# Kernel optimization log

Measured on AMD Instinct MI355X. Metric: run time of the kernel, lower is better.

Reference implementation:

```python
import jax, jax.numpy as jnp
import numpy as np

N, F, T, E = 20000, 128, 4, 640000
TBL = 10002  # oscillator lookup: indices 0..10001 (clamped inputs map to 10001)
EPS = 1e-5


def setup_inputs() -> dict:
    key = jax.random.key(0)
    ks = jax.random.split(key, 12)
    rn = lambda k, shp, s: (jax.random.normal(k, shp, dtype=jnp.float32) * s)
    return {
        "x": rn(ks[0], (N, F), 1.0),
        "osc_table": jax.random.uniform(ks[1], (TBL,), dtype=jnp.float32),
        "edge_index": jax.random.randint(ks[2], (2, E), 0, N, dtype=jnp.int32),
        "edge_type": jax.random.randint(ks[3], (E,), 0, T, dtype=jnp.int32),
        "w_ih": rn(ks[4], (4 * F, F), 0.05),
        "w_hh": rn(ks[5], (4 * F, F), 0.05),
        "b_ih": jnp.zeros((4 * F,), jnp.float32),
        "b_hh": jnp.zeros((4 * F,), jnp.float32),
        "conv1_w": rn(ks[6], (T, 2 * F, F), 0.001),
        "conv1_b": jnp.zeros((2 * F,), jnp.float32),
        "conv2_w": rn(ks[7], (T, F, 2 * F), 0.001),
        "conv2_b": jnp.zeros((F,), jnp.float32),
        "lin1_w": rn(ks[8], (2 * F, F), 0.05),
        "lin1_b": jnp.zeros((2 * F,), jnp.float32),
        "lin2_w": rn(ks[9], (F, 2 * F), 0.05),
        "lin2_b": jnp.zeros((F,), jnp.float32),
        "bn1_g": jnp.ones((2 * F,), jnp.float32),
        "bn1_b": jnp.zeros((2 * F,), jnp.float32),
        "bn2_g": jnp.ones((F,), jnp.float32),
        "bn2_b": jnp.zeros((F,), jnp.float32),
    }


def _oscillator(x, table):
    # clamp out-of-range inputs to 0.5001 -> index 10001
    xi = jnp.where((x < -0.5) | (x > 0.5), jnp.float32(0.5001), x)
    idx = jnp.floor((xi + 0.5) * 10000.0).astype(jnp.int32)
    vals = table[idx]
    # where table value is 0, fall back to Sig'(original input) = sigmoid(x) (s=1)
    return jnp.where(vals == 0, jax.nn.sigmoid(x), vals)


def _ec_conv(x, W, b, src, dst, etype):
    # per-edge-type scatter-MAX aggregation, vectorized via composite segment ids
    msgs = x[src]                                  # [E, Cin]
    seg = dst * T + etype                          # [E]
    agg = jax.ops.segment_max(msgs, seg, num_segments=N * T)  # [N*T, Cin]
    agg = jnp.where(jnp.isfinite(agg), agg, 0.0)   # empty segments (-inf) -> 0 (PyG zero-fill)
    agg = agg.reshape(N, T, -1)
    # sum_t linear(agg_t, W_t, b) ; bias is added once per edge type in the torch loop
    return jnp.einsum("ntc,toc->no", agg, W) + T * b


def _batchnorm(x, gamma, beta):
    mu = jnp.mean(x, axis=0)
    var = jnp.mean((x - mu) ** 2, axis=0)          # biased variance (training mode)
    return (x - mu) * jax.lax.rsqrt(var + EPS) * gamma + beta


def reference(x, osc_table, edge_index, edge_type, w_ih, w_hh, b_ih, b_hh,
              conv1_w, conv1_b, conv2_w, conv2_b, lin1_w, lin1_b, lin2_w, lin2_b,
              bn1_g, bn1_b, bn2_g, bn2_b):
    src, dst = edge_index[0], edge_index[1]
    h = _oscillator(x, osc_table)
    # LSTM over a length-1 sequence (unsqueeze(0), batch_first=False) with zero state:
    gates = h @ w_ih.T + b_ih + b_hh               # h0=0 so w_hh contributes nothing
    i, f, g, o = jnp.split(gates, 4, axis=-1)
    c = jax.nn.sigmoid(i) * jnp.tanh(g)
    h = jax.nn.sigmoid(o) * jnp.tanh(c)
    h = h @ lin1_w.T + lin1_b + _ec_conv(h, conv1_w, conv1_b, src, dst, edge_type)
    h = jax.nn.relu(_batchnorm(h, bn1_g, bn1_b))
    h = h @ lin2_w.T + lin2_b + _ec_conv(h, conv2_w, conv2_b, src, dst, edge_type)
    h = _batchnorm(h, bn2_g, bn2_b)
    return jax.nn.sigmoid(h - 10.0)
```

## Files before the change

### kernel.cpp

```cpp
#include <hip/hip_runtime.h>
#include <math.h>

#define NN 20000
#define NE 640000
#define TT 4
#define FF 128
#define FF2 256
#define NSEG (NN*TT)
#define MP 20096
#define NBUCK 157
#define EPSBN 1e-5f

typedef short bf16x8 __attribute__((ext_vector_type(8)));
typedef float f32x4  __attribute__((ext_vector_type(4)));
typedef unsigned short us2 __attribute__((ext_vector_type(2)));

__device__ __forceinline__ float sigf(float x){ return 1.0f/(1.0f+expf(-x)); }

__device__ __forceinline__ unsigned short f2bf(float x){
  union { float f; unsigned u; } v; v.f = x;
  unsigned r = v.u + 0x7FFF + ((v.u >> 16) & 1);
  return (unsigned short)(r >> 16);
}
__device__ __forceinline__ float bf2f(unsigned short u){
  union { float f; unsigned u; } v; v.u = ((unsigned)u) << 16; return v.f;
}

__device__ __forceinline__ unsigned char f2f8(float x){
  union{float f; unsigned u;} v; v.f = x;
  unsigned s = (v.u >> 24) & 0x80u;
  unsigned a = v.u & 0x7FFFFFFFu;
  if(a > 0x43E00000u) a = 0x43E00000u;
  union{unsigned u; float f;} w; w.u = a;
  float ax = w.f;
  if(ax < 0.015625f){
    int q = (int)rintf(ax * 512.0f);
    return (unsigned char)(s | (unsigned)q);
  }
  unsigned rb = a & 0xFFFFFu;
  unsigned base = a >> 20;
  unsigned r = base + (((rb > 0x80000u) || (rb == 0x80000u && (base & 1u))) ? 1u : 0u);
  unsigned e = r >> 3, m3 = r & 7u;
  int fe = (int)e - 120;
  if(fe >= 16) return (unsigned char)(s | 0x7Eu);
  return (unsigned char)(s | ((unsigned)fe << 3) | m3);
}
__device__ __forceinline__ unsigned char fold8(unsigned char b){
  return (unsigned char)(b ^ ((b & 0x80u) ? 0xFFu : 0x80u));
}
__device__ __forceinline__ unsigned short key8tobf(unsigned char k){
  unsigned char b = (unsigned char)(k ^ ((k & 0x80u) ? 0x80u : 0xFFu));
  unsigned s = ((unsigned)b & 0x80u) << 24;
  unsigned e = ((unsigned)b >> 3) & 0xFu;
  unsigned m = (unsigned)b & 7u;
  union{unsigned u; float f;} v;
  if(e == 0){ v.f = (float)m * 0.001953125f; v.u |= s; }
  else v.u = s | ((e + 120u) << 23) | (m << 20);
  return (unsigned short)(v.u >> 16);
}
__device__ __forceinline__ void acc8(unsigned v, unsigned &me, unsigned &mo){
  union U{unsigned u; us2 v;};
  U a, b, r;
  a.u = __builtin_amdgcn_perm(v, 0u, 0x0C060C04u);
  b.u = me; r.v = __builtin_elementwise_max(a.v, b.v); me = r.u;
  a.u = __builtin_amdgcn_perm(v, 0u, 0x0C070C05u);
  b.u = mo; r.v = __builtin_elementwise_max(a.v, b.v); mo = r.u;
}
__device__ __forceinline__ unsigned maxsplit(unsigned a, unsigned b){
  union U{unsigned u; us2 v;};
  U x, y, r; x.u = a; y.u = b;
  r.v = __builtin_elementwise_max(x.v, y.v);
  return r.u;
}

#define PB0 147456
#define PB1 (PB0 + 229376)
#define PB2 (PB1 + 229376)
__global__ __launch_bounds__(256)
void k_prep(const float* __restrict__ w_ih, const float* __restrict__ lin1_w,
            const float* __restrict__ conv1_w, const float* __restrict__ lin2_w,
            const float* __restrict__ conv2_w,
            const float* __restrict__ bih, const float* __restrict__ bhh,
            const float* __restrict__ l1b, const float* __restrict__ c1b,
            const float* __restrict__ l2b, const float* __restrict__ c2b,
            unsigned short* __restrict__ Bp0, unsigned short* __restrict__ Bp1,
            unsigned short* __restrict__ Bp2,
            float* __restrict__ bias0, float* __restrict__ bias1, float* __restrict__ bias2,
            int* __restrict__ gbcnt, int* __restrict__ gcursor,
            float* __restrict__ bnsum1, float* __restrict__ bnsum2){
  int gi = blockIdx.x*256 + threadIdx.x;
  if(gi < PB0){
    int k = gi/384, o = gi - k*384;
    int grow = (o < 128) ? o : o + 128;
    int reg = k >> 7, c = k & 127;
    float w = w_ih[(size_t)grow*128 + c];
    unsigned short hu = f2bf(w);
    Bp0[((size_t)(k >> 3)*384 + o)*8 + (k & 7)] = (reg == 1) ? f2bf(w - bf2f(hu)) : hu;
  } else if(gi < PB1){
    int i = gi - PB0; int k = i >> 8, o = i & 255;
    int reg = k >> 7;
    unsigned short val;
    if(reg < 3){
      float w = lin1_w[(size_t)o*128 + (k & 127)];
      unsigned short hu = f2bf(w);
      val = (reg == 1) ? f2bf(w - bf2f(hu)) : hu;
    } else {
      int kk = k - 384; int t = kk >> 7; int c = kk & 127;
      val = f2bf(conv1_w[((size_t)t*256 + o)*128 + c]);
    }
    Bp1[((size_t)(k >> 3)*256 + o)*8 + (k & 7)] = val;
  } else if(gi < PB2){
    int i = gi - PB1; int k = i >> 7, o = i & 127;
    int reg = k >> 8;
    unsigned short val;
    if(reg < 3){
      float w = lin2_w[(size_t)o*256 + (k & 255)];
      unsigned short hu = f2bf(w);
      val = (reg == 1) ? f2bf(w - bf2f(hu)) : hu;
    } else {
      int kk = k - 768; int t = kk >> 8; int c = kk & 255;
      val = f2bf(conv2_w[((size_t)t*128 + o)*256 + c]);
    }
    Bp2[((size_t)(k >> 3)*128 + o)*8 + (k & 7)] = val;
  } else {
    int t = gi - PB2;
    if(t < 384){ int grow = (t < 128) ? t : t + 128; bias0[t] = bih[grow] + bhh[grow]; }
    else if(t < 640){ int c = t - 384; bias1[c] = l1b[c] + 4.0f*c1b[c]; }
    else if(t < 768){ int c = t - 640; bias2[c] = l2b[c] + 4.0f*c2b[c]; }
    else if(t < 1280){ bnsum1[t - 768] = 0.0f; }
    else if(t < 1536){ bnsum2[t - 1280] = 0.0f; }
    else if(t < 1536 + NBUCK){ gbcnt[t - 1536] = 0; }
    else if(t < 1536 + 2*NBUCK){ gcursor[t - 1536 - NBUCK] = 0; }
  }
}

__global__ void k_osc_pack(const float* __restrict__ x, const float* __restrict__ tbl,
                           unsigned short* __restrict__ A0){
  int i = blockIdx.x*256 + threadIdx.x;
  if(i >= NN*FF) return;
  int n = i >> 7, j = i & 127;
  float xv = x[i];
  float xi = (xv < -0.5f || xv > 0.5f) ? 0.5001f : xv;
  int idx = (int)floorf((xi + 0.5f) * 10000.0f);
  float tv = tbl[idx];
  float hv = (tv == 0.0f) ? sigf(xv) : tv;
  unsigned short hu = f2bf(hv);
  unsigned short lu = f2bf(hv - bf2f(hu));
  unsigned short* r = A0 + (size_t)n*256;
  r[j] = hu; r[128+j] = lu;
}

template<int C, int COUT, int SPLITS, int AK>
__global__ __launch_bounds__(256)
void k_gemm(const unsigned short* __restrict__ A, const unsigned short* __restrict__ Bp,
            float* __restrict__ out){
  int w  = threadIdx.x >> 6;
  int l  = threadIdx.x & 63;
  int wr = w >> 1, wc = w & 1;
  int lr = l & 15, lg = l >> 4;
  int n0 = blockIdx.x*128 + wr*64;
  int c0 = blockIdx.y*128 + wc*64;
  constexpr int Q = (AK + C)/SPLITS;
  int zq0 = blockIdx.z*Q, zq1 = zq0 + Q;
  int kb = (zq0 <= 2*C) ? (zq0 >> 1) : (zq0 - C);
  int ke = (zq1 <= 2*C) ? (zq1 >> 1) : (zq1 - C);
  const size_t abase = (size_t)(n0 + lr)*AK + lg*8;
  const size_t bstep = (size_t)COUT*8;
  const unsigned short* bcolp = Bp + (size_t)(c0 + lr)*8 + lg*bstep;
  f32x4 acc[4][4] = {};
  int kde = ke < C ? ke : C;
  for(int ak = kb; ak < kde; ak += 32){
    bf16x8 a[4];
    #pragma unroll
    for(int r = 0; r < 4; ++r) a[r] = *(const bf16x8*)(A + abase + (size_t)r*16*AK + ak);
    const unsigned short* p1 = bcolp + (size_t)(ak >> 3)*bstep;
    const unsigned short* p2 = bcolp + (size_t)((C + ak) >> 3)*bstep;
    #pragma unroll
    for(int j = 0; j < 4; ++j){
      bf16x8 b1 = *(const bf16x8*)(p1 + j*128);
      bf16x8 b2 = *(const bf16x8*)(p2 + j*128);
      #pragma unroll
      for(int r = 0; r < 4; ++r){
        acc[r][j] = __builtin_amdgcn_mfma_f32_16x16x32_bf16(a[r], b1, acc[r][j], 0, 0, 0);
        acc[r][j] = __builtin_amdgcn_mfma_f32_16x16x32_bf16(a[r], b2, acc[r][j], 0, 0, 0);
      }
    }
  }
  int ks = kb > C ? kb : C;
  for(int ak = ks; ak < ke; ak += 32){
    bf16x8 a[4];
    #pragma unroll
    for(int r = 0; r < 4; ++r) a[r] = *(const bf16x8*)(A + abase + (size_t)r*16*AK + ak);
    const unsigned short* p = bcolp + (size_t)((C + ak) >> 3)*bstep;
    #pragma unroll
    for(int j = 0; j < 4; ++j){
      bf16x8 b = *(const bf16x8*)(p + j*128);
      #pragma unroll
      for(int r = 0; r < 4; ++r)
        acc[r][j] = __builtin_amdgcn_mfma_f32_16x16x32_bf16(a[r], b, acc[r][j], 0, 0, 0);
    }
  }
  float* o = out + (size_t)blockIdx.z*NN*COUT;
  #pragma unroll
  for(int r = 0; r < 4; ++r){
    int nb = n0 + r*16 + lg*4;
    #pragma unroll
    for(int j = 0; j < 4; ++j){
      int oc = c0 + j*16 + lr;
      #pragma unroll
      for(int q = 0; q < 4; ++q){
        int n = nb + q;
        if(n < NN) o[(size_t)n*COUT + oc] = acc[r][j][q];
      }
    }
  }
}

template<int COUT, int SPLITS>
__global__ __launch_bounds__(COUT)
void k_reduce(const float* __restrict__ P, const float* __restrict__ bias,
              float* __restrict__ h, float* __restrict__ sums){
  int c = threadIdx.x;
  float bs = bias[c];
  float s = 0.0f, s2 = 0.0f;
  for(int n = blockIdx.x; n < NN; n += gridDim.x){
    float v = bs;
    #pragma unroll
    for(int z = 0; z < SPLITS; ++z) v += P[(size_t)z*NN*COUT + (size_t)n*COUT + c];
    h[(size_t)n*COUT + c] = v;
    s += v; s2 += v*v;
  }
  atomicAdd(&sums[c], s);
  atomicAdd(&sums[COUT + c], s2);
}

__global__ void k_act(const float* __restrict__ gates, const float* __restrict__ bias0,
                      unsigned short* __restrict__ A1, unsigned char* __restrict__ h1k8){
  int i = blockIdx.x*256 + threadIdx.x;
  if(i >= NN*FF) return;
  int n = i >> 7, j = i & 127;
  const float* g = gates + (size_t)n*384;
  float ig = g[j]       + bias0[j];
  float gg = g[128 + j] + bias0[128 + j];
  float og = g[256 + j] + bias0[256 + j];
  float c  = sigf(ig) * tanhf(gg);
  float hv = sigf(og) * tanhf(c);
  unsigned short hu = f2bf(hv);
  unsigned short lu = f2bf(hv - bf2f(hu));
  unsigned short* r = A1 + (size_t)n*768;
  r[j] = hu; r[128 + j] = lu;
  h1k8[i] = fold8(f2f8(hv));
}

__global__ void k_bcount(const int* __restrict__ dst, int* __restrict__ gbcnt){
  __shared__ int h[NBUCK];
  for(int i = threadIdx.x; i < NBUCK; i += 256) h[i] = 0;
  __syncthreads();
  int e0 = blockIdx.x*2048;
  #pragma unroll
  for(int k = 0; k < 8; ++k){
    int e = e0 + threadIdx.x + k*256;
    if(e < NE) atomicAdd(&h[dst[e] >> 7], 1);
  }
  __syncthreads();
  for(int i = threadIdx.x; i < NBUCK; i += 256) if(h[i]) atomicAdd(&gbcnt[i], h[i]);
}
__global__ void k_bscan(const int* __restrict__ gbcnt, int* __restrict__ gbase,
                        int* __restrict__ excl){
  if(threadIdx.x == 0){
    int s = 0;
    for(int i = 0; i < NBUCK; ++i){ gbase[i] = s; s += gbcnt[i]; }
    excl[NSEG] = s;
  }
}
__global__ __launch_bounds__(512)
void k_binscat(const int* __restrict__ src, const int* __restrict__ dst,
               const int* __restrict__ et, const int* __restrict__ gbase,
               int* __restrict__ gcursor, unsigned* __restrict__ gstage){
  __shared__ unsigned stage[4096];
  __shared__ unsigned char stgb[4096];
  __shared__ int lcnt[NBUCK], lexc[NBUCK], lcur[NBUCK], gofs[NBUCK];
  __shared__ int s2[256];
  int tid = threadIdx.x;
  for(int i = tid; i < NBUCK; i += 512) lcnt[i] = 0;
  __syncthreads();
  int e0 = blockIdx.x*4096;
  int b_[8]; unsigned v_[8];
  #pragma unroll
  for(int k = 0; k < 8; ++k){
    int e = e0 + tid + k*512;
    if(e < NE){
      int d = dst[e]; int b = d >> 7;
      b_[k] = b;
      v_[k] = ((unsigned)((((d & 127) << 2) | et[e])) << 16) | (unsigned)src[e];
      atomicAdd(&lcnt[b], 1);
    } else b_[k] = -1;
  }
  __syncthreads();
  if(tid < 256) s2[tid] = (tid < NBUCK) ? lcnt[tid] : 0;
  __syncthreads();
  for(int off = 1; off < 256; off <<= 1){
    int add = (tid < 256 && tid >= off) ? s2[tid - off] : 0;
    __syncthreads();
    if(tid < 256) s2[tid] += add;
    __syncthreads();
  }
  if(tid < NBUCK) lexc[tid] = s2[tid] - lcnt[tid];
  __syncthreads();
  if(tid < NBUCK){
    lcur[tid] = lexc[tid];
    if(lcnt[tid]) gofs[tid] = atomicAdd(&gcursor[tid], lcnt[tid]);
  }
  __syncthreads();
  #pragma unroll
  for(int k = 0; k < 8; ++k){
    if(b_[k] >= 0){
      int p = atomicAdd(&lcur[b_[k]], 1);
      stage[p] = v_[k]; stgb[p] = (unsigned char)b_[k];
    }
  }
  __syncthreads();
  int ne = NE - e0; if(ne > 4096) ne = 4096;
  for(int i = tid; i < ne; i += 512){
    int b = stgb[i];
    gstage[gbase[b] + gofs[b] + (i - lexc[b])] = stage[i];
  }
}
__global__ __launch_bounds__(512)
void k_fine(const unsigned* __restrict__ gstage, const int* __restrict__ gbcnt,
            const int* __restrict__ gbase, int* __restrict__ excl,
            unsigned short* __restrict__ elist){
  __shared__ int cnt[512], scn[512], cur[512];
  int t = threadIdx.x, bk = blockIdx.x;
  cnt[t] = 0;
  __syncthreads();
  int gB = gbase[bk], cE = gbcnt[bk];
  for(int i = t; i < cE; i += 512) atomicAdd(&cnt[gstage[gB + i] >> 16], 1);
  __syncthreads();
  scn[t] = cnt[t]; __syncthreads();
  for(int off = 1; off < 512; off <<= 1){
    int add = (t >= off) ? scn[t - off] : 0;
    __syncthreads();
    scn[t] += add;
    __syncthreads();
  }
  int ex = scn[t] - cnt[t];
  cur[t] = ex;
  int s = bk*512 + t;
  if(s < NSEG) excl[s] = gB + ex;
  __syncthreads();
  for(int i = t; i < cE; i += 512){
    unsigned v = gstage[gB + i];
    int p = atomicAdd(&cur[v >> 16], 1);
    elist[gB + p] = (unsigned short)(v & 0xFFFFu);
  }
}

template<int C, int AK>
__global__ __launch_bounds__(256)
void k_agg8(const unsigned char* __restrict__ keys, const unsigned short* __restrict__ elist,
            const int* __restrict__ excl, unsigned short* __restrict__ A){
  constexpr int NW = C/128;
  __shared__ unsigned short slut[256];
  if(threadIdx.x < 256) slut[threadIdx.x] = key8tobf((unsigned char)threadIdx.x);
  __syncthreads();
  int seg  = blockIdx.x*4 + (threadIdx.x >> 6);
  int l = threadIdx.x & 63, half = l >> 5, cl = l & 31;
  int start = excl[seg];
  int cnt   = excl[seg + 1] - start;
  const unsigned char* kp = keys + cl*(NW*4);
  unsigned me0 = 0, mo0 = 0, me1 = 0, mo1 = 0;
  for(int bb = 0; bb < cnt; bb += 64){
    int m = cnt - bb; if(m > 64) m = 64;
    int ee = (int)elist[start + bb + l];
    int k = 0;
    for(; k + 8 <= m; k += 8){
      int e0 = __shfl(ee, k + half);
      int e1 = __shfl(ee, k + 2 + half);
      int e2 = __shfl(ee, k + 4 + half);
      int e3 = __shfl(ee, k + 6 + half);
      if constexpr(NW == 1){
        unsigned v0 = *(const unsigned*)(kp + (size_t)e0*C);
        unsigned v1 = *(const unsigned*)(kp + (size_t)e1*C);
        unsigned v2 = *(const unsigned*)(kp + (size_t)e2*C);
        unsigned v3 = *(const unsigned*)(kp + (size_t)e3*C);
        acc8(v0, me0, mo0); acc8(v1, me0, mo0);
        acc8(v2, me0, mo0); acc8(v3, me0, mo0);
      } else {
        uint2 v0 = *(const uint2*)(kp + (size_t)e0*C);
        uint2 v1 = *(const uint2*)(kp + (size_t)e1*C);
        uint2 v2 = *(const uint2*)(kp + (size_t)e2*C);
        uint2 v3 = *(const uint2*)(kp + (size_t)e3*C);
        acc8(v0.x, me0, mo0); acc8(v0.y, me1, mo1);
        acc8(v1.x, me0, mo0); acc8(v1.y, me1, mo1);
        acc8(v2.x, me0, mo0); acc8(v2.y, me1, mo1);
        acc8(v3.x, me0, mo0); acc8(v3.y, me1, mo1);
      }
    }
    for(; k + 2 <= m; k += 2){
      int e = __shfl(ee, k + half);
      if constexpr(NW == 1){
        acc8(*(const unsigned*)(kp + (size_t)e*C), me0, mo0);
      } else {
        uint2 v = *(const uint2*)(kp + (size_t)e*C);
        acc8(v.x, me0, mo0); acc8(v.y, me1, mo1);
      }
    }
    if(k < m){
      int e = __shfl(ee, k);
      if(half == 0){
        if constexpr(NW == 1){
          acc8(*(const unsigned*)(kp + (size_t)e*C), me0, mo0);
        } else {
          uint2 v = *(const uint2*)(kp + (size_t)e*C);
          acc8(v.x, me0, mo0); acc8(v.y, me1, mo1);
        }
      }
    }
  }
  me0 = maxsplit(me0, (unsigned)__shfl_xor((int)me0, 32));
  mo0 = maxsplit(mo0, (unsigned)__shfl_xor((int)mo0, 32));
  if constexpr(NW == 2){
    me1 = maxsplit(me1, (unsigned)__shfl_xor((int)me1, 32));
    mo1 = maxsplit(mo1, (unsigned)__shfl_xor((int)mo1, 32));
  }
  if(half == 0){
    int n = seg >> 2, t = seg & 3;
    unsigned short* op = A + (size_t)n*AK + 2*C + t*C + cl*(NW*4);
    if constexpr(NW == 1){
      typedef unsigned short u4 __attribute__((ext_vector_type(4)));
      u4 o;
      o[0] = cnt ? slut[me0 & 0xFF] : (unsigned short)0;
      o[1] = cnt ? slut[mo0 & 0xFF] : (unsigned short)0;
      o[2] = cnt ? slut[(me0 >> 16) & 0xFF] : (unsigned short)0;
      o[3] = cnt ? slut[(mo0 >> 16) & 0xFF] : (unsigned short)0;
      *(u4*)op = o;
    } else {
      typedef unsigned short u8v __attribute__((ext_vector_type(8)));
      u8v o;
      o[0] = cnt ? slut[me0 & 0xFF] : (unsigned short)0;
      o[1] = cnt ? slut[mo0 & 0xFF] : (unsigned short)0;
      o[2] = cnt ? slut[(me0 >> 16) & 0xFF] : (unsigned short)0;
      o[3] = cnt ? slut[(mo0 >> 16) & 0xFF] : (unsigned short)0;
      o[4] = cnt ? slut[me1 & 0xFF] : (unsigned short)0;
      o[5] = cnt ? slut[mo1 & 0xFF] : (unsigned short)0;
      o[6] = cnt ? slut[(me1 >> 16) & 0xFF] : (unsigned short)0;
      o[7] = cnt ? slut[(mo1 >> 16) & 0xFF] : (unsigned short)0;
      *(u8v*)op = o;
    }
  }
}

__global__ void k_bnrp(const float* __restrict__ h2, const float* __restrict__ sums,
                       const float* __restrict__ g, const float* __restrict__ bb,
                       unsigned short* __restrict__ A2, unsigned char* __restrict__ h2k8){
  int i = blockIdx.x*256 + threadIdx.x;
  if(i >= NN*FF2) return;
  int n = i >> 8, c = i & 255;
  float mean = sums[c] * (1.0f/NN);
  float var  = sums[256 + c] * (1.0f/NN) - mean*mean;
  float scale = g[c] / sqrtf(var + EPSBN);
  float shift = bb[c] - mean*scale;
  float v = fmaxf(h2[i]*scale + shift, 0.0f);
  unsigned short hu = f2bf(v);
  unsigned short lu = f2bf(v - bf2f(hu));
  unsigned short* r = A2 + (size_t)n*1536;
  r[c] = hu; r[256 + c] = lu;
  h2k8[i] = fold8(f2f8(v));
}

__global__ void k_bnsig(float* __restrict__ h, const float* __restrict__ sums,
                        const float* __restrict__ g, const float* __restrict__ bb){
  int i = blockIdx.x*256 + threadIdx.x;
  if(i >= NN*FF) return;
  int c = i & 127;
  float mean = sums[c] * (1.0f/NN);
  float var  = sums[128 + c] * (1.0f/NN) - mean*mean;
  float scale = g[c] / sqrtf(var + EPSBN);
  float shift = bb[c] - mean*scale;
  float v = h[i]*scale + shift - 10.0f;
  h[i] = 1.0f/(1.0f + expf(-v));
}

extern "C" void kernel_launch(void* const* d_in, const int* in_sizes, int n_in,
                              void* d_out, int out_size, void* d_ws, size_t ws_size,
                              hipStream_t stream){
  (void)in_sizes; (void)n_in; (void)out_size; (void)ws_size;
  const float* x       = (const float*)d_in[0];
  const float* tbl     = (const float*)d_in[1];
  const int*   eidx    = (const int*)  d_in[2];
  const int*   etype   = (const int*)  d_in[3];
  const float* w_ih    = (const float*)d_in[4];
  const float* b_ih    = (const float*)d_in[6];
  const float* b_hh    = (const float*)d_in[7];
  const float* conv1_w = (const float*)d_in[8];
  const float* conv1_b = (const float*)d_in[9];
  const float* conv2_w = (const float*)d_in[10];
  const float* conv2_b = (const float*)d_in[11];
  const float* lin1_w  = (const float*)d_in[12];
  const float* lin1_b  = (const float*)d_in[13];
  const float* lin2_w  = (const float*)d_in[14];
  const float* lin2_b  = (const float*)d_in[15];
  const float* bn1_g   = (const float*)d_in[16];
  const float* bn1_b   = (const float*)d_in[17];
  const float* bn2_g   = (const float*)d_in[18];
  const float* bn2_b   = (const float*)d_in[19];
  float* out = (float*)d_out;

  char* base = (char*)d_ws;
  size_t off = 0;
  auto alloc = [&](size_t bytes){ char* p = base + off; off = (off + bytes + 255) & ~(size_t)255; return p; };

  unsigned short* A0 = (unsigned short*)alloc((size_t)MP * 256 * 2);
  unsigned short* A1 = (unsigned short*)alloc((size_t)MP * 768 * 2);
  unsigned short* A2 = (unsigned short*)alloc((size_t)MP * 1536 * 2);
  float* h2raw = (float*)alloc((size_t)NN * 256 * 4);
  unsigned char* h1k8 = (unsigned char*)alloc((size_t)NN * 128);
  unsigned char* h2k8 = (unsigned char*)alloc((size_t)NN * 256);
  unsigned short* Bp0 = (unsigned short*)alloc((size_t)384 * 384 * 2);
  unsigned short* Bp1 = (unsigned short*)alloc((size_t)896 * 256 * 2);
  unsigned short* Bp2 = (unsigned short*)alloc((size_t)1792 * 128 * 2);
  float* bias0 = (float*)alloc(384 * 4);
  float* bias1 = (float*)alloc(256 * 4);
  float* bias2 = (float*)alloc(128 * 4);
  int* excl    = (int*)alloc((NSEG + 1) * 4);
  float* bnsum1 = (float*)alloc(512 * 4);
  float* bnsum2 = (float*)alloc(256 * 4);
  int* gbcnt   = (int*)alloc(NBUCK * 4);
  int* gbase   = (int*)alloc(NBUCK * 4);
  int* gcursor = (int*)alloc(NBUCK * 4);
  unsigned* gstage = (unsigned*)alloc((size_t)NE * 4);
  unsigned short* elist = (unsigned short*)alloc((size_t)NE * 2 + 256);

  float* gates = (float*)A2;
  float* P1    = (float*)A2;
  float* P2    = (float*)A0;

  const int* src = eidx;
  const int* dst = eidx + NE;

  k_prep<<<(PB2 + 1850 + 255)/256, 256, 0, stream>>>(
      w_ih, lin1_w, conv1_w, lin2_w, conv2_w,
      b_ih, b_hh, lin1_b, conv1_b, lin2_b, conv2_b,
      Bp0, Bp1, Bp2, bias0, bias1, bias2, gbcnt, gcursor, bnsum1, bnsum2);

  k_osc_pack<<<(NN*FF + 255)/256, 256, 0, stream>>>(x, tbl, A0);

  k_bcount<<<(NE + 2047)/2048, 256, 0, stream>>>(dst, gbcnt);
  k_bscan<<<1, 64, 0, stream>>>(gbcnt, gbase, excl);
  k_binscat<<<(NE + 4095)/4096, 512, 0, stream>>>(src, dst, etype, gbase, gcursor, gstage);
  k_fine<<<NBUCK, 512, 0, stream>>>(gstage, gbcnt, gbase, excl, elist);

  k_gemm<128, 384, 1, 256><<<dim3(157, 3, 1), 256, 0, stream>>>(A0, Bp0, gates);
  k_act<<<(NN*FF + 255)/256, 256, 0, stream>>>(gates, bias0, A1, h1k8);

  k_agg8<128, 768><<<NSEG/4, 256, 0, stream>>>(h1k8, elist, excl, A1);
  k_gemm<128, 256, 2, 768><<<dim3(157, 2, 2), 256, 0, stream>>>(A1, Bp1, P1);
  k_reduce<256, 2><<<256, 256, 0, stream>>>(P1, bias1, h2raw, bnsum1);
  k_bnrp<<<(NN*FF2 + 255)/256, 256, 0, stream>>>(h2raw, bnsum1, bn1_g, bn1_b, A2, h2k8);

  k_agg8<256, 1536><<<NSEG/4, 256, 0, stream>>>(h2k8, elist, excl, A2);
  k_gemm<256, 128, 4, 1536><<<dim3(157, 1, 4), 256, 0, stream>>>(A2, Bp2, P2);
  k_reduce<128, 4><<<256, 128, 0, stream>>>(P2, bias2, out, bnsum2);
  k_bnsig<<<(NN*FF + 255)/256, 256, 0, stream>>>(out, bnsum2, bn2_g, bn2_b);
}
```

Measured before the change: 275.0 us.

## Merge prep, oscillator and bucket-count kernels; store split-K partials as bf16

Folds weight packing, the oscillator/pack step and the destination bucket histogram into a single launch that picks its role by block index. Zeroing of the BN sums and bucket counters moves to a hipMemsetAsync over a contiguous buffer region. The split-K GEMM partials for both conv layers are now written as bf16 instead of fp32, halving partial-sum traffic into the reduce kernels. The trade is precision: the partial sums are rounded to bf16 before being added and fed into batchnorm.

Result: no change. 277.9 us (+1.0%).

```diff
diff --git a/kernel.cpp b/kernel.cpp
--- a/kernel.cpp
+++ b/kernel.cpp
@@ -76,84 +76,98 @@
 #define PB0 147456
 #define PB1 (PB0 + 229376)
 #define PB2 (PB1 + 229376)
+#define NB_PREP ((PB2 + 768 + 255)/256)
+#define NB_OSC  ((NN*FF + 255)/256)
+#define NB_CNT  ((NE + 2047)/2048)
 __global__ __launch_bounds__(256)
-void k_prep(const float* __restrict__ w_ih, const float* __restrict__ lin1_w,
-            const float* __restrict__ conv1_w, const float* __restrict__ lin2_w,
-            const float* __restrict__ conv2_w,
-            const float* __restrict__ bih, const float* __restrict__ bhh,
-            const float* __restrict__ l1b, const float* __restrict__ c1b,
-            const float* __restrict__ l2b, const float* __restrict__ c2b,
-            unsigned short* __restrict__ Bp0, unsigned short* __restrict__ Bp1,
-            unsigned short* __restrict__ Bp2,
-            float* __restrict__ bias0, float* __restrict__ bias1, float* __restrict__ bias2,
-            int* __restrict__ gbcnt, int* __restrict__ gcursor,
-            float* __restrict__ bnsum1, float* __restrict__ bnsum2){
-  int gi = blockIdx.x*256 + threadIdx.x;
-  if(gi < PB0){
-    int k = gi/384, o = gi - k*384;
-    int grow = (o < 128) ? o : o + 128;
-    int reg = k >> 7, c = k & 127;
-    float w = w_ih[(size_t)grow*128 + c];
-    unsigned short hu = f2bf(w);
-    Bp0[((size_t)(k >> 3)*384 + o)*8 + (k & 7)] = (reg == 1) ? f2bf(w - bf2f(hu)) : hu;
-  } else if(gi < PB1){
-    int i = gi - PB0; int k = i >> 8, o = i & 255;
-    int reg = k >> 7;
-    unsigned short val;
-    if(reg < 3){
-      float w = lin1_w[(size_t)o*128 + (k & 127)];
+void k_front(const float* __restrict__ w_ih, const float* __restrict__ lin1_w,
+             const float* __restrict__ conv1_w, const float* __restrict__ lin2_w,
+             const float* __restrict__ conv2_w,
+             const float* __restrict__ bih, const float* __restrict__ bhh,
+             const float* __restrict__ l1b, const float* __restrict__ c1b,
+             const float* __restrict__ l2b, const float* __restrict__ c2b,
+             unsigned short* __restrict__ Bp0, unsigned short* __restrict__ Bp1,
+             unsigned short* __restrict__ Bp2,
+             float* __restrict__ bias0, float* __restrict__ bias1, float* __restrict__ bias2,
+             const float* __restrict__ x, const float* __restrict__ tbl,
+             unsigned short* __restrict__ A0,
+             const int* __restrict__ dst, int* __restrict__ gbcnt){
+  __shared__ int h[NBUCK];
+  int bid = blockIdx.x;
+  if(bid < NB_PREP){
+    int gi = bid*256 + threadIdx.x;
+    if(gi < PB0){
+      int k = gi/384, o = gi - k*384;
+      int grow = (o < 128) ? o : o + 128;
+      int reg = k >> 7, c = k & 127;
+      float w = w_ih[(size_t)grow*128 + c];
       unsigned short hu = f2bf(w);
-      val = (reg == 1) ? f2bf(w - bf2f(hu)) : hu;
+      Bp0[((size_t)(k >> 3)*384 + o)*8 + (k & 7)] = (reg == 1) ? f2bf(w - bf2f(hu)) : hu;
+    } else if(gi < PB1){
+      int i = gi - PB0; int k = i >> 8, o = i & 255;
+      int reg = k >> 7;
+      unsigned short val;
+      if(reg < 3){
+        float w = lin1_w[(size_t)o*128 + (k & 127)];
+        unsigned short hu = f2bf(w);
+        val = (reg == 1) ? f2bf(w - bf2f(hu)) : hu;
+      } else {
+        int kk = k - 384; int t = kk >> 7; int c = kk & 127;
+        val = f2bf(conv1_w[((size_t)t*256 + o)*128 + c]);
+      }
+      Bp1[((size_t)(k >> 3)*256 + o)*8 + (k & 7)] = val;
+    } else if(gi < PB2){
+      int i = gi - PB1; int k = i >> 7, o = i & 127;
+      int reg = k >> 8;
+      unsigned short val;
+      if(reg < 3){
+        float w = lin2_w[(size_t)o*256 + (k & 255)];
+        unsigned short hu = f2bf(w);
+        val = (reg == 1) ? f2bf(w - bf2f(hu)) : hu;
+      } else {
+        int kk = k - 768; int t = kk >> 8; int c = kk & 255;
+        val = f2bf(conv2_w[((size_t)t*128 + o)*256 + c]);
+      }
+      Bp2[((size_t)(k >> 3)*128 + o)*8 + (k & 7)] = val;
     } else {
-      int kk = k - 384; int t = kk >> 7; int c = kk & 127;
-      val = f2bf(conv1_w[((size_t)t*256 + o)*128 + c]);
-    }
-    Bp1[((size_t)(k >> 3)*256 + o)*8 + (k & 7)] = val;
-  } else if(gi < PB2){
-    int i = gi - PB1; int k = i >> 7, o = i & 127;
-    int reg = k >> 8;
-    unsigned short val;
-    if(reg < 3){
-      float w = lin2_w[(size_t)o*256 + (k & 255)];
-      unsigned short hu = f2bf(w);
-      val = (reg == 1) ? f2bf(w - bf2f(hu)) : hu;
-    } else {
-      int kk = k - 768; int t = kk >> 8; int c = kk & 255;
-      val = f2bf(conv2_w[((size_t)t*128 + o)*256 + c]);
-    }
-    Bp2[((size_t)(k >> 3)*128 + o)*8 + (k & 7)] = val;
+      int t = gi - PB2;
+      if(t < 384){ int grow = (t < 128) ? t : t + 128; bias0[t] = bih[grow] + bhh[grow]; }
+      else if(t < 640){ int c = t - 384; bias1[c] = l1b[c] + 4.0f*c1b[c]; }
+      else if(t < 768){ int c = t - 640; bias2[c] = l2b[c] + 4.0f*c2b[c]; }
+    }
+  } else if(bid < NB_PREP + NB_OSC){
+    int i = (bid - NB_PREP)*256 + threadIdx.x;
+    if(i < NN*FF){
+      int n = i >> 7, j = i & 127;
+      float xv = x[i];
+      float xi = (xv < -0.5f || xv > 0.5f) ? 0.5001f : xv;
+      int idx = (int)floorf((xi + 0.5f) * 10000.0f);
+      float tv = tbl[idx];
+      float hv = (tv == 0.0f) ? sigf(xv) : tv;
+      unsigned short hu = f2bf(hv);
+      unsigned short lu = f2bf(hv - bf2f(hu));
+      unsigned short* r = A0 + (size_t)n*256;
+      r[j] = hu; r[128+j] = lu;
+    }
   } else {
-    int t = gi - PB2;
-    if(t < 384){ int grow = (t < 128) ? t : t + 128; bias0[t] = bih[grow] + bhh[grow]; }
-    else if(t < 640){ int c = t - 384; bias1[c] = l1b[c] + 4.0f*c1b[c]; }
-    else if(t < 768){ int c = t - 640; bias2[c] = l2b[c] + 4.0f*c2b[c]; }
-    else if(t < 1280){ bnsum1[t - 768] = 0.0f; }
-    else if(t < 1536){ bnsum2[t - 1280] = 0.0f; }
-    else if(t < 1536 + NBUCK){ gbcnt[t - 1536] = 0; }
-    else if(t < 1536 + 2*NBUCK){ gcursor[t - 1536 - NBUCK] = 0; }
-  }
-}
-
-__global__ void k_osc_pack(const float* __restrict__ x, const float* __restrict__ tbl,
-                           unsigned short* __restrict__ A0){
-  int i = blockIdx.x*256 + threadIdx.x;
-  if(i >= NN*FF) return;
-  int n = i >> 7, j = i & 127;
-  float xv = x[i];
-  float xi = (xv < -0.5f || xv > 0.5f) ? 0.5001f : xv;
-  int idx = (int)floorf((xi + 0.5f) * 10000.0f);
-  float tv = tbl[idx];
-  float hv = (tv == 0.0f) ? sigf(xv) : tv;
-  unsigned short hu = f2bf(hv);
-  unsigned short lu = f2bf(hv - bf2f(hu));
-  unsigned short* r = A0 + (size_t)n*256;
-  r[j] = hu; r[128+j] = lu;
-}
-
-template<int C, int COUT, int SPLITS, int AK>
+    int cb = bid - NB_PREP - NB_OSC;
+    for(int i = threadIdx.x; i < NBUCK; i += 256) h[i] = 0;
+    __syncthreads();
+    int e0 = cb*2048;
+    #pragma unroll
+    for(int k = 0; k < 8; ++k){
+      int e = e0 + threadIdx.x + k*256;
+      if(e < NE) atomicAdd(&h[dst[e] >> 7], 1);
+    }
+    __syncthreads();
+    for(int i = threadIdx.x; i < NBUCK; i += 256) if(h[i]) atomicAdd(&gbcnt[i], h[i]);
+  }
+}
+
+template<int C, int COUT, int SPLITS, int AK, bool B16OUT>
 __global__ __launch_bounds__(256)
 void k_gemm(const unsigned short* __restrict__ A, const unsigned short* __restrict__ Bp,
-            float* __restrict__ out){
+            void* __restrict__ outv){
   int w  = threadIdx.x >> 6;
   int l  = threadIdx.x & 63;
   int wr = w >> 1, wc = w & 1;
@@ -200,7 +214,6 @@
         acc[r][j] = __builtin_amdgcn_mfma_f32_16x16x32_bf16(a[r], b, acc[r][j], 0, 0, 0);
     }
   }
-  float* o = out + (size_t)blockIdx.z*NN*COUT;
   #pragma unroll
   for(int r = 0; r < 4; ++r){
     int nb = n0 + r*16 + lg*4;
@@ -210,7 +223,15 @@
       #pragma unroll
       for(int q = 0; q < 4; ++q){
         int n = nb + q;
-        if(n < NN) o[(size_t)n*COUT + oc] = acc[r][j][q];
+        if(n < NN){
+          if constexpr(B16OUT){
+            unsigned short* o = (unsigned short*)outv + (size_t)blockIdx.z*NN*COUT;
+            o[(size_t)n*COUT + oc] = f2bf(acc[r][j][q]);
+          } else {
+            float* o = (float*)outv + (size_t)blockIdx.z*NN*COUT;
+            o[(size_t)n*COUT + oc] = acc[r][j][q];
+          }
+        }
       }
     }
   }
@@ -218,7 +239,7 @@
 
 template<int COUT, int SPLITS>
 __global__ __launch_bounds__(COUT)
-void k_reduce(const float* __restrict__ P, const float* __restrict__ bias,
+void k_reduce(const unsigned short* __restrict__ P, const float* __restrict__ bias,
               float* __restrict__ h, float* __restrict__ sums){
   int c = threadIdx.x;
   float bs = bias[c];
@@ -226,7 +247,7 @@
   for(int n = blockIdx.x; n < NN; n += gridDim.x){
     float v = bs;
     #pragma unroll
-    for(int z = 0; z < SPLITS; ++z) v += P[(size_t)z*NN*COUT + (size_t)n*COUT + c];
+    for(int z = 0; z < SPLITS; ++z) v += bf2f(P[(size_t)z*NN*COUT + (size_t)n*COUT + c]);
     h[(size_t)n*COUT + c] = v;
     s += v; s2 += v*v;
   }
@@ -252,19 +273,6 @@
   h1k8[i] = fold8(f2f8(hv));
 }
 
-__global__ void k_bcount(const int* __restrict__ dst, int* __restrict__ gbcnt){
-  __shared__ int h[NBUCK];
-  for(int i = threadIdx.x; i < NBUCK; i += 256) h[i] = 0;
-  __syncthreads();
-  int e0 = blockIdx.x*2048;
-  #pragma unroll
-  for(int k = 0; k < 8; ++k){
-    int e = e0 + threadIdx.x + k*256;
-    if(e < NE) atomicAdd(&h[dst[e] >> 7], 1);
-  }
-  __syncthreads();
-  for(int i = threadIdx.x; i < NBUCK; i += 256) if(h[i]) atomicAdd(&gbcnt[i], h[i]);
-}
 __global__ void k_bscan(const int* __restrict__ gbcnt, int* __restrict__ gbase,
                         int* __restrict__ excl){
   if(threadIdx.x == 0){
@@ -527,40 +535,41 @@
   float* bnsum1 = (float*)alloc(512 * 4);
   float* bnsum2 = (float*)alloc(256 * 4);
   int* gbcnt   = (int*)alloc(NBUCK * 4);
+  int* gcursor = (int*)alloc(NBUCK * 4);
+  size_t zbytes = (size_t)((char*)(gcursor + NBUCK) - (char*)bnsum1);
   int* gbase   = (int*)alloc(NBUCK * 4);
-  int* gcursor = (int*)alloc(NBUCK * 4);
   unsigned* gstage = (unsigned*)alloc((size_t)NE * 4);
   unsigned short* elist = (unsigned short*)alloc((size_t)NE * 2 + 256);
 
   float* gates = (float*)A2;
-  float* P1    = (float*)A2;
-  float* P2    = (float*)A0;
+  unsigned short* P1 = (unsigned short*)A2;
+  unsigned short* P2 = (unsigned short*)A0;
 
   const int* src = eidx;
   const int* dst = eidx + NE;
 
-  k_prep<<<(PB2 + 1850 + 255)/256, 256, 0, stream>>>(
+  hipMemsetAsync(bnsum1, 0, zbytes, stream);
+
+  k_front<<<NB_PREP + NB_OSC + NB_CNT, 256, 0, stream>>>(
       w_ih, lin1_w, conv1_w, lin2_w, conv2_w,
       b_ih, b_hh, lin1_b, conv1_b, lin2_b, conv2_b,
-      Bp0, Bp1, Bp2, bias0, bias1, bias2, gbcnt, gcursor, bnsum1, bnsum2);
-
-  k_osc_pack<<<(NN*FF + 255)/256, 256, 0, stream>>>(x, tbl, A0);
-
-  k_bcount<<<(NE + 2047)/2048, 256, 0, stream>>>(dst, gbcnt);
+      Bp0, Bp1, Bp2, bias0, bias1, bias2,
+      x, tbl, A0, dst, gbcnt);
+
   k_bscan<<<1, 64, 0, stream>>>(gbcnt, gbase, excl);
   k_binscat<<<(NE + 4095)/4096, 512, 0, stream>>>(src, dst, etype, gbase, gcursor, gstage);
   k_fine<<<NBUCK, 512, 0, stream>>>(gstage, gbcnt, gbase, excl, elist);
 
-  k_gemm<128, 384, 1, 256><<<dim3(157, 3, 1), 256, 0, stream>>>(A0, Bp0, gates);
+  k_gemm<128, 384, 1, 256, false><<<dim3(157, 3, 1), 256, 0, stream>>>(A0, Bp0, gates);
   k_act<<<(NN*FF + 255)/256, 256, 0, stream>>>(gates, bias0, A1, h1k8);
 
   k_agg8<128, 768><<<NSEG/4, 256, 0, stream>>>(h1k8, elist, excl, A1);
-  k_gemm<128, 256, 2, 768><<<dim3(157, 2, 2), 256, 0, stream>>>(A1, Bp1, P1);
+  k_gemm<128, 256, 2, 768, true><<<dim3(157, 2, 2), 256, 0, stream>>>(A1, Bp1, P1);
   k_reduce<256, 2><<<256, 256, 0, stream>>>(P1, bias1, h2raw, bnsum1);
   k_bnrp<<<(NN*FF2 + 255)/256, 256, 0, stream>>>(h2raw, bnsum1, bn1_g, bn1_b, A2, h2k8);
 
   k_agg8<256, 1536><<<NSEG/4, 256, 0, stream>>>(h2k8, elist, excl, A2);
-  k_gemm<256, 128, 4, 1536><<<dim3(157, 1, 4), 256, 0, stream>>>(A2, Bp2, P2);
+  k_gemm<256, 128, 4, 1536, true><<<dim3(157, 1, 4), 256, 0, stream>>>(A2, Bp2, P2);
   k_reduce<128, 4><<<256, 128, 0, stream>>>(P2, bias2, out, bnsum2);
   k_bnsig<<<(NN*FF + 255)/256, 256, 0, stream>>>(out, bnsum2, bn2_g, bn2_b);
 }
```
